# Kernel optimization log

Hardware: AMD Instinct MI355X
Metric: run time of the kernel (lower is better)

Reference implementation:

```python
import jax, jax.numpy as jnp
import numpy as np

N = 50000   # nodes
E = 600000  # edges
IN = 512    # in_channels
H = 128     # hidden_channels
B = 64      # graphs in batch
L = 4       # GatedGraphConv layers
VIEWS = [[0, 9, 10], [1, 2, 3], [4, 5, 6], [7, 8, 11, 12]]  # syntactic/sequential/semantic/discourse


def layer_norm(x, w, b, eps=1e-5):
    mu = x.mean(-1, keepdims=True)
    var = ((x - mu) ** 2).mean(-1, keepdims=True)
    return (x - mu) / jnp.sqrt(var + eps) * w + b


def setup_inputs() -> dict:
    key = jax.random.key(0)
    ks = jax.random.split(key, 32)
    p = lambda k, shape: (jax.random.normal(k, shape, jnp.float32) * 0.02)
    inp = {
        'x': jax.random.normal(ks[0], (N, IN), jnp.float32),
        'edge_index': jax.random.randint(ks[1], (2, E), 0, N, dtype=jnp.int32),
        'edge_type': jax.random.randint(ks[2], (E,), 0, 13, dtype=jnp.int32),
        'batch': jnp.sort(jax.random.randint(ks[3], (N,), 0, B, dtype=jnp.int32)),
        # input projection (Linear + LayerNorm)
        'proj_w': p(ks[4], (IN, H)), 'proj_b': p(ks[5], (H,)),
        'ln0_w': jnp.ones((H,), jnp.float32), 'ln0_b': jnp.zeros((H,), jnp.float32),
        # per-view GatedGraphConv: weight [views, layers, H, H] + GRUCell params [views, 3H, H]
        'ggnn_w': p(ks[6], (4, L, H, H)),
        'gru_wih': p(ks[7], (4, 3 * H, H)), 'gru_whh': p(ks[8], (4, 3 * H, H)),
        'gru_bih': p(ks[9], (4, 3 * H)), 'gru_bhh': p(ks[10], (4, 3 * H)),
        # per-view LayerNorm
        'vln_w': jnp.ones((4, H), jnp.float32), 'vln_b': jnp.zeros((4, H), jnp.float32),
        # attention fusion
        'q_w': p(ks[11], (H, H)), 'q_b': p(ks[12], (H,)),
        'k_w': p(ks[13], (H, H)), 'k_b': p(ks[14], (H,)),
        # classifier MLP: 2H -> H -> H//2 -> 1
        'c1_w': p(ks[15], (2 * H, H)), 'c1_b': p(ks[16], (H,)),
        'c2_w': p(ks[17], (H, H // 2)), 'c2_b': p(ks[18], (H // 2,)),
        'c3_w': p(ks[19], (H // 2, 1)), 'c3_b': p(ks[20], (1,)),
    }
    return inp


def reference(x, edge_index, edge_type, batch, proj_w, proj_b, ln0_w, ln0_b,
              ggnn_w, gru_wih, gru_whh, gru_bih, gru_bhh, vln_w, vln_b,
              q_w, q_b, k_w, k_b, c1_w, c1_b, c2_w, c2_b, c3_w, c3_b):
    # input projection: Linear -> LayerNorm -> GELU (dropout = identity in eval)
    h0 = jax.nn.gelu(layer_norm(x @ proj_w + proj_b, ln0_w, ln0_b), approximate=False)
    src, dst = edge_index[0], edge_index[1]
    views = []
    for v in range(4):
        emask = jnp.zeros((E,), bool)
        for t in VIEWS[v]:
            emask = emask | (edge_type == t)
        em = emask.astype(h0.dtype)[:, None]  # [E,1] edge-type view mask
        h = h0
        for i in range(L):
            m = h @ ggnn_w[v, i]                                   # [N,H]
            agg = jax.ops.segment_sum(m[src] * em, dst, num_segments=N)  # masked scatter-add
            # GRUCell(input=agg, hidden=h), torch gate order r,z,n
            gi = agg @ gru_wih[v].T + gru_bih[v]
            gh = h @ gru_whh[v].T + gru_bhh[v]
            ir, iz, inn = jnp.split(gi, 3, -1)
            hr, hz, hn = jnp.split(gh, 3, -1)
            r = jax.nn.sigmoid(ir + hr)
            z = jax.nn.sigmoid(iz + hz)
            n = jnp.tanh(inn + r * hn)
            h = (1.0 - z) * n + z * h
        views.append(layer_norm(h, vln_w[v], vln_b[v]) + h0)  # residual ViewEncoder
    hs = jnp.stack(views, 1)  # [N,4,H]
    # node-conditioned attention fusion
    q = jnp.tanh(h0 @ q_w + q_b)
    keys = hs @ k_w + k_b
    attn = jax.nn.softmax(jnp.einsum('nh,nvh->nv', q, keys) * (H ** -0.5), axis=-1)
    fused = jnp.einsum('nvh,nv->nh', hs, attn)
    # global mean + max pooling per graph
    cnt = jax.ops.segment_sum(jnp.ones((N,), fused.dtype), batch, num_segments=B)
    x_mean = jax.ops.segment_sum(fused, batch, num_segments=B) / jnp.maximum(cnt, 1.0)[:, None]
    x_max = jax.ops.segment_max(fused, batch, num_segments=B)
    g = jnp.concatenate([x_mean, x_max], -1)  # [B,2H]
    h1 = jax.nn.relu(g @ c1_w + c1_b)
    h2 = jax.nn.relu(h1 @ c2_w + c2_b)
    return h2 @ c3_w + c3_b  # [B,1] logits
```

## Files before the change

kernel.cpp:

```cpp
#include <hip/hip_runtime.h>
#include <math.h>


typedef __attribute__((ext_vector_type(8))) short short8;
typedef __attribute__((ext_vector_type(4))) float floatx4;

__device__ __forceinline__ unsigned short f2bf_rtn(float x) {
    unsigned u = __float_as_uint(x);
    return (unsigned short)((u + 0x7FFFu + ((u >> 16) & 1u)) >> 16);
}
__device__ __forceinline__ float bf2f(unsigned short h) {
    return __uint_as_float((unsigned)h << 16);
}
__device__ __forceinline__ float fsig(float x) {
    return __builtin_amdgcn_rcpf(1.0f + __expf(-x));
}
__device__ __forceinline__ float ftanh(float x) {
    return 1.0f - 2.0f * __builtin_amdgcn_rcpf(__expf(2.0f * x) + 1.0f);
}

__device__ __forceinline__ int view_of(int t) {
    return (t >= 1 && t <= 3) ? 1 : (t >= 4 && t <= 6) ? 2
         : ((t == 7) || (t == 8) || (t >= 11)) ? 3 : 0;
}

template <bool BT, int EPI>
__global__ __launch_bounds__(256, 2) void gemm_k(
    const float* __restrict__ A, const float* __restrict__ Bm,
    const float* __restrict__ bias, float* __restrict__ C,
    int N, int M, int K, long sA, long sB, long sC)
{
    __shared__ float As[32][132];
    __shared__ float Bs[32][132];
    A  += (long)blockIdx.z * sA;
    Bm += (long)blockIdx.z * sB;
    C  += (long)blockIdx.z * sC;
    const int r0 = blockIdx.x * 128;
    const int c0 = blockIdx.y * 128;
    const int tid = threadIdx.x;
    const int tx = tid & 15;
    const int ty = tid >> 4;

    float acc[8][8];
#pragma unroll
    for (int i = 0; i < 8; i++)
#pragma unroll
        for (int j = 0; j < 8; j++) acc[i][j] = 0.0f;

    for (int k0 = 0; k0 < K; k0 += 32) {
        {
            int arow = tid >> 3;
            int akq  = (tid & 7) << 2;
#pragma unroll
            for (int hh = 0; hh < 4; hh++) {
                int r  = arow + hh * 32;
                int gr = r0 + r;
                float4 av = make_float4(0.f, 0.f, 0.f, 0.f);
                if (gr < N) av = *(const float4*)(A + (long)gr * K + k0 + akq);
                As[akq + 0][r] = av.x; As[akq + 1][r] = av.y;
                As[akq + 2][r] = av.z; As[akq + 3][r] = av.w;
            }
        }
        if (BT) {
            int brow = tid >> 3;
            int bkq  = (tid & 7) << 2;
#pragma unroll
            for (int hh = 0; hh < 4; hh++) {
                int r = brow + hh * 32;
                float4 bv = *(const float4*)(Bm + (long)(c0 + r) * K + k0 + bkq);
                Bs[bkq + 0][r] = bv.x; Bs[bkq + 1][r] = bv.y;
                Bs[bkq + 2][r] = bv.z; Bs[bkq + 3][r] = bv.w;
            }
        } else {
            int kk0 = tid >> 5;
            int bmq = (tid & 31) << 2;
#pragma unroll
            for (int hh = 0; hh < 4; hh++) {
                int kk = kk0 + hh * 8;
                float4 bv = *(const float4*)(Bm + (long)(k0 + kk) * M + c0 + bmq);
                *(float4*)&Bs[kk][bmq] = bv;
            }
        }
        __syncthreads();
#pragma unroll
        for (int k = 0; k < 32; k++) {
            float4 a0 = *(const float4*)&As[k][ty << 2];
            float4 a1 = *(const float4*)&As[k][64 + (ty << 2)];
            float4 b0 = *(const float4*)&Bs[k][tx << 2];
            float4 b1 = *(const float4*)&Bs[k][64 + (tx << 2)];
            float av[8] = {a0.x, a0.y, a0.z, a0.w, a1.x, a1.y, a1.z, a1.w};
            float bv[8] = {b0.x, b0.y, b0.z, b0.w, b1.x, b1.y, b1.z, b1.w};
#pragma unroll
            for (int i = 0; i < 8; i++)
#pragma unroll
                for (int j = 0; j < 8; j++) acc[i][j] += av[i] * bv[j];
        }
        __syncthreads();
    }

    float bb[8] = {0, 0, 0, 0, 0, 0, 0, 0};
    if (bias) {
        float4 b0 = *(const float4*)(bias + c0 + (tx << 2));
        float4 b1 = *(const float4*)(bias + c0 + 64 + (tx << 2));
        bb[0] = b0.x; bb[1] = b0.y; bb[2] = b0.z; bb[3] = b0.w;
        bb[4] = b1.x; bb[5] = b1.y; bb[6] = b1.z; bb[7] = b1.w;
    }
#pragma unroll
    for (int i = 0; i < 8; i++) {
        int r = (i < 4) ? (r0 + (ty << 2) + i) : (r0 + 64 + (ty << 2) + i - 4);
        if (r < N) {
            float v[8];
#pragma unroll
            for (int j = 0; j < 8; j++) {
                v[j] = acc[i][j] + bb[j];
                if (EPI == 1) v[j] = tanhf(v[j]);
            }
            *(float4*)(C + (long)r * M + c0 + (tx << 2)) = make_float4(v[0], v[1], v[2], v[3]);
            *(float4*)(C + (long)r * M + c0 + 64 + (tx << 2)) = make_float4(v[4], v[5], v[6], v[7]);
        }
    }
}

__global__ __launch_bounds__(256) void build_p_k(
    const float* __restrict__ gwih, const float* __restrict__ gwhh,
    const float* __restrict__ gbih, const float* __restrict__ gbhh,
    float* __restrict__ pih, float* __restrict__ phh, float* __restrict__ bp)
{
    int idx = blockIdx.x * 256 + threadIdx.x;
    if (idx < 16 * 65536) {
        int z = idx >> 16, rem = idx & 65535;
        int k = rem >> 9, mcol = rem & 511;
        int ch = mcol >> 2, g = mcol & 3;
        int v = z >> 2;
        const float* Wih = gwih + (long)v * 384 * 128;
        float val = 0.0f;
        if (g == 0) val = Wih[ch * 128 + k];
        else if (g == 1) val = Wih[(128 + ch) * 128 + k];
        else if (g == 2) val = Wih[(256 + ch) * 128 + k];
        pih[idx] = val;
    }
    if (idx < 4 * 65536) {
        int v = idx >> 16, rem = idx & 65535;
        int k = rem >> 9, mcol = rem & 511;
        int ch = mcol >> 2, g = mcol & 3;
        const float* Whh = gwhh + (long)v * 384 * 128;
        float val = 0.0f;
        if (g == 0) val = Whh[ch * 128 + k];
        else if (g == 1) val = Whh[(128 + ch) * 128 + k];
        else if (g == 3) val = Whh[(256 + ch) * 128 + k];
        phh[idx] = val;
    }
    if (idx < 4 * 512) {
        int v = idx >> 9, mcol = idx & 511;
        int ch = mcol >> 2, g = mcol & 3;
        float val;
        if (g == 0) val = gbih[v * 384 + ch] + gbhh[v * 384 + ch];
        else if (g == 1) val = gbih[v * 384 + 128 + ch] + gbhh[v * 384 + 128 + ch];
        else if (g == 2) val = gbih[v * 384 + 256 + ch];
        else val = gbhh[v * 384 + 256 + ch];
        bp[idx] = val;
    }
}

__global__ __launch_bounds__(256) void pack_b_k(
    const float* __restrict__ wcomb, const float* __restrict__ phh,
    short* __restrict__ Bp)
{
    int idx = blockIdx.x * 256 + threadIdx.x;
    if (idx >= 16 * 256 * 512) return;
    int z = idx >> 17, rem = idx & 131071;
    int k = rem >> 9, col = rem & 511;
    int g  = col & 3;
    int q  = (col >> 2) & 3;
    int tn = (col >> 4) & 7;
    int ch = ((col >> 7) << 5) + (q << 3) + tn;
    int mcol = (ch << 2) + g;
    float val = (k < 128) ? wcomb[(long)z * 65536 + k * 512 + mcol]
                          : phh[(long)(z >> 2) * 65536 + (k - 128) * 512 + mcol];
    long dst = ((long)(z * 8 + (k >> 5)) * 512 + col) * 32 + ((k >> 3) & 3) * 8 + (k & 7);
    Bp[dst] = (short)f2bf_rtn(val);
}

template <bool BT>
__global__ __launch_bounds__(256) void pack_w_k(
    const float* __restrict__ W, short* __restrict__ bhi, short* __restrict__ blo, int K)
{
    int idx = blockIdx.x * 256 + threadIdx.x;
    if (idx >= K * 128) return;
    int k = idx >> 7, col = idx & 127;
    float v = BT ? W[col * K + k] : W[k * 128 + col];
    unsigned short h = f2bf_rtn(v);
    float fh = __uint_as_float((unsigned)h << 16);
    long dst = ((long)(k >> 5) * 128 + col) * 32 + ((k >> 3) & 3) * 8 + (k & 7);
    bhi[dst] = (short)h;
    blo[dst] = (short)f2bf_rtn(v - fh);
}

template <int EPI>
__global__ __launch_bounds__(256, 4) void gemm_mfma_k(
    const float* __restrict__ A, const short* __restrict__ Bhi,
    const short* __restrict__ Blo, const float* __restrict__ bias,
    float* __restrict__ C, int N, int K)
{
    __shared__ __align__(16) short Ahi[64 * 40];
    __shared__ __align__(16) short Alo[64 * 40];
    const int r0 = blockIdx.x * 64;
    const int tid = threadIdx.x;
    const int l = tid & 63, w = tid >> 6;
    const int wrow = w * 16;
    const int m = l & 15, q = l >> 4;

    floatx4 acc[8];
#pragma unroll
    for (int b = 0; b < 8; b++) acc[b] = (floatx4)0.0f;

    const int arow = tid >> 2;
    const int fcol = (tid & 3) * 8;
    const int gr = r0 + arow;
    const int nks = K >> 5;

    for (int ks = 0; ks < nks; ks++) {
        float xv[8];
        if (gr < N) {
            float4 x0 = *(const float4*)(A + (long)gr * K + ks * 32 + fcol);
            float4 x1 = *(const float4*)(A + (long)gr * K + ks * 32 + fcol + 4);
            xv[0] = x0.x; xv[1] = x0.y; xv[2] = x0.z; xv[3] = x0.w;
            xv[4] = x1.x; xv[5] = x1.y; xv[6] = x1.z; xv[7] = x1.w;
        } else {
#pragma unroll
            for (int u = 0; u < 8; u++) xv[u] = 0.0f;
        }
        short8 vhi, vlo;
#pragma unroll
        for (int u = 0; u < 8; u++) {
            unsigned short hb = f2bf_rtn(xv[u]);
            float fh = __uint_as_float((unsigned)hb << 16);
            vhi[u] = (short)hb;
            vlo[u] = (short)f2bf_rtn(xv[u] - fh);
        }
        *(short8*)&Ahi[arow * 40 + fcol] = vhi;
        *(short8*)&Alo[arow * 40 + fcol] = vlo;
        __syncthreads();
        short8 ah = *(short8*)&Ahi[(wrow + m) * 40 + q * 8];
        short8 al = *(short8*)&Alo[(wrow + m) * 40 + q * 8];
#pragma unroll
        for (int tn = 0; tn < 8; tn++) {
            int col = tn * 16 + m;
            short8 bh = *(const short8*)(Bhi + ((long)ks * 128 + col) * 32 + q * 8);
            short8 bl = *(const short8*)(Blo + ((long)ks * 128 + col) * 32 + q * 8);
            acc[tn] = __builtin_amdgcn_mfma_f32_16x16x32_bf16(ah, bh, acc[tn], 0, 0, 0);
            acc[tn] = __builtin_amdgcn_mfma_f32_16x16x32_bf16(al, bh, acc[tn], 0, 0, 0);
            acc[tn] = __builtin_amdgcn_mfma_f32_16x16x32_bf16(ah, bl, acc[tn], 0, 0, 0);
        }
        __syncthreads();
    }

#pragma unroll
    for (int tn = 0; tn < 8; tn++) {
        int col = tn * 16 + m;
        float bb = bias ? bias[col] : 0.0f;
#pragma unroll
        for (int reg = 0; reg < 4; reg++) {
            int row = r0 + wrow + q * 4 + reg;
            if (row < N) {
                float v = acc[tn][reg] + bb;
                if (EPI == 1) v = ftanh(v);
                C[(long)row * 128 + col] = v;
            }
        }
    }
}

__global__ __launch_bounds__(512, 4) void gemm_gru_mfma_k(
    const short* __restrict__ hb, const short* __restrict__ hpHi,
    const short* __restrict__ hpLo, const short* __restrict__ Bp,
    const float* __restrict__ bp, short* __restrict__ outHi,
    short* __restrict__ outLo, const int* __restrict__ off,
    const int* __restrict__ esrc, int N, long sV, long sHb, long sHp)
{
    __shared__ __align__(16) short As[8 * 64 * 40];
    const int x = blockIdx.x;
    const int z = blockIdx.z;
    const short* hbz = hb + (long)z * sHb;
    const short* hph = hpHi + (long)z * sHp;
    const short* hpl = hpLo + (long)z * sHp;
    Bp  += (long)z * 524288;
    bp  += (long)z * 512;
    outHi += (long)z * sV;
    outLo += (long)z * sV;
    const int r0  = x * 64;
    const int tid = threadIdx.x;
    const int l = tid & 63, w = tid >> 6;
    const int wrow = (w & 1) * 32, wcol = (w >> 1) * 128;
    const int m = l & 15, q = l >> 4;

    const int row8 = tid >> 3;
    const int cg8  = tid & 7;
    const int gr = r0 + row8;

    {
        float accS[16];
#pragma unroll
        for (int u = 0; u < 16; u++) accS[u] = 0.0f;
        if (gr < N) {
            const int idx = z * N + gr;
            int j = off[idx];
            const int end = off[idx + 1];
            if (j < end) {
                const short* sp = hb + (long)esrc[j] * 128 + (cg8 << 4);
                short8 p0 = *(const short8*)(sp);
                short8 p1 = *(const short8*)(sp + 8);
                for (; j < end;) {
                    short8 c0 = p0, c1 = p1;
                    ++j;
                    if (j < end) {
                        const short* sq = hb + (long)esrc[j] * 128 + (cg8 << 4);
                        p0 = *(const short8*)(sq);
                        p1 = *(const short8*)(sq + 8);
                    }
#pragma unroll
                    for (int u = 0; u < 8; u++) {
                        accS[u]     += bf2f((unsigned short)c0[u]);
                        accS[8 + u] += bf2f((unsigned short)c1[u]);
                    }
                }
            }
        }
        short8 o0, o1;
#pragma unroll
        for (int u = 0; u < 8; u++) {
            o0[u] = (short)f2bf_rtn(accS[u]);
            o1[u] = (short)f2bf_rtn(accS[8 + u]);
        }
        const int base = (cg8 >> 1) * 2560 + row8 * 40 + (cg8 & 1) * 16;
        *(short8*)&As[base]     = o0;
        *(short8*)&As[base + 8] = o1;
    }

    {
        short8 h0v = (short8)0, h1v = (short8)0;
        if (gr < N) {
            const short* hp = hbz + (long)gr * 128 + (cg8 << 4);
            h0v = *(const short8*)(hp);
            h1v = *(const short8*)(hp + 8);
        }
        const int base = (4 + (cg8 >> 1)) * 2560 + row8 * 40 + (cg8 & 1) * 16;
        *(short8*)&As[base]     = h0v;
        *(short8*)&As[base + 8] = h1v;
    }
    __syncthreads();

    floatx4 acc[2][8];
#pragma unroll
    for (int a = 0; a < 2; a++)
#pragma unroll
        for (int b = 0; b < 8; b++) acc[a][b] = (floatx4)0.0f;

#pragma unroll
    for (int ks = 0; ks < 8; ks++) {
        short8 bfr[8];
#pragma unroll
        for (int tn = 0; tn < 8; tn++) {
            int col = wcol + tn * 16 + m;
            bfr[tn] = *(const short8*)(Bp + ((long)ks * 512 + col) * 32 + q * 8);
        }
        short8 a0 = *(short8*)&As[ks * 2560 + (wrow + m) * 40 + q * 8];
        short8 a1 = *(short8*)&As[ks * 2560 + (wrow + 16 + m) * 40 + q * 8];
#pragma unroll
        for (int tn = 0; tn < 8; tn++) {
            acc[0][tn] = __builtin_amdgcn_mfma_f32_16x16x32_bf16(bfr[tn], a0, acc[0][tn], 0, 0, 0);
            acc[1][tn] = __builtin_amdgcn_mfma_f32_16x16x32_bf16(bfr[tn], a1, acc[1][tn], 0, 0, 0);
        }
    }

    const int chq = (wcol >> 2) + q * 8;
#pragma unroll
    for (int a = 0; a < 2; a++) {
        const int row = r0 + wrow + a * 16 + m;
        if (row < N) {
            short8 h8 = *(const short8*)(hph + (long)row * 128 + chq);
            short8 l8 = *(const short8*)(hpl + (long)row * 128 + chq);
            float hnv[8];
            short8 ohi, olo;
#pragma unroll
            for (int tn = 0; tn < 8; tn++) {
                float hp = bf2f((unsigned short)h8[tn]) + bf2f((unsigned short)l8[tn]);
                float4 bv = *(const float4*)(bp + (chq + tn) * 4);
                floatx4 A = acc[a][tn];
                float rr = fsig(A[0] + bv.x);
                float zz = fsig(A[1] + bv.y);
                float nn = ftanh(A[2] + bv.z + rr * (A[3] + bv.w));
                hnv[tn] = (1.0f - zz) * nn + zz * hp;
                unsigned short hh = f2bf_rtn(hnv[tn]);
                ohi[tn] = (short)hh;
                olo[tn] = (short)f2bf_rtn(hnv[tn] - bf2f(hh));
            }
            *(short8*)(outHi + (long)row * 128 + chq) = ohi;
            *(short8*)(outLo + (long)row * 128 + chq) = olo;
        }
    }
}

__global__ __launch_bounds__(256) void ln_gelu_k(
    float* __restrict__ h0, short* __restrict__ h0b, short* __restrict__ h0lo,
    const float* __restrict__ w, const float* __restrict__ b, int N)
{
    long t = (long)blockIdx.x * 256 + threadIdx.x;
    int n = (int)(t >> 5), lane = (int)(t & 31);
    if (n >= N) return;
    float* p = h0 + (long)n * 128 + lane * 4;
    float4 x = *(float4*)p;
    float s = x.x + x.y + x.z + x.w;
#pragma unroll
    for (int off = 16; off >= 1; off >>= 1) s += __shfl_xor(s, off);
    float mu = s * (1.0f / 128.0f);
    float4 d = make_float4(x.x - mu, x.y - mu, x.z - mu, x.w - mu);
    float ss = d.x * d.x + d.y * d.y + d.z * d.z + d.w * d.w;
#pragma unroll
    for (int off = 16; off >= 1; off >>= 1) ss += __shfl_xor(ss, off);
    float inv = 1.0f / sqrtf(ss * (1.0f / 128.0f) + 1e-5f);
    float4 wv = *(const float4*)(w + lane * 4);
    float4 bv = *(const float4*)(b + lane * 4);
    float y[4] = {d.x * inv * wv.x + bv.x, d.y * inv * wv.y + bv.y,
                  d.z * inv * wv.z + bv.z, d.w * inv * wv.w + bv.w};
#pragma unroll
    for (int i = 0; i < 4; i++)
        y[i] = 0.5f * y[i] * (1.0f + erff(y[i] * 0.70710678118654752f));
    *(float4*)p = make_float4(y[0], y[1], y[2], y[3]);
    ushort4 hb, lb;
    hb.x = f2bf_rtn(y[0]); lb.x = f2bf_rtn(y[0] - bf2f(hb.x));
    hb.y = f2bf_rtn(y[1]); lb.y = f2bf_rtn(y[1] - bf2f(hb.y));
    hb.z = f2bf_rtn(y[2]); lb.z = f2bf_rtn(y[2] - bf2f(hb.z));
    hb.w = f2bf_rtn(y[3]); lb.w = f2bf_rtn(y[3] - bf2f(hb.w));
    *(ushort4*)(h0b + (long)n * 128 + lane * 4) = hb;
    *(ushort4*)(h0lo + (long)n * 128 + lane * 4) = lb;
}

__global__ __launch_bounds__(256) void count_k(
    const int* __restrict__ dst, const int* __restrict__ et,
    int* __restrict__ cnt, int E, int N)
{
    int e = blockIdx.x * 256 + threadIdx.x;
    if (e >= E) return;
    int v = view_of(et[e]);
    atomicAdd(&cnt[v * N + dst[e]], 1);
}

__global__ __launch_bounds__(256) void scan1_k(
    const int* __restrict__ cnt, int* __restrict__ off, int* __restrict__ bsum, int n)
{
    __shared__ int sm[256];
    int base = blockIdx.x * 1024;
    int tid = threadIdx.x;
    int v[4]; int s = 0;
#pragma unroll
    for (int i = 0; i < 4; i++) {
        int idx = base + tid * 4 + i;
        v[i] = (idx < n) ? cnt[idx] : 0; s += v[i];
    }
    sm[tid] = s; __syncthreads();
    for (int o = 1; o < 256; o <<= 1) {
        int t2 = (tid >= o) ? sm[tid - o] : 0;
        __syncthreads(); sm[tid] += t2; __syncthreads();
    }
    int run = sm[tid] - s;
    if (tid == 255) bsum[blockIdx.x] = sm[255];
#pragma unroll
    for (int i = 0; i < 4; i++) {
        int idx = base + tid * 4 + i;
        if (idx < n) off[idx] = run;
        run += v[i];
    }
}

__global__ __launch_bounds__(256) void scan2_k(int* __restrict__ bsum, int nb)
{
    __shared__ int sm[256];
    int tid = threadIdx.x;
    int v = (tid < nb) ? bsum[tid] : 0;
    sm[tid] = v; __syncthreads();
    for (int o = 1; o < 256; o <<= 1) {
        int t2 = (tid >= o) ? sm[tid - o] : 0;
        __syncthreads(); sm[tid] += t2; __syncthreads();
    }
    if (tid < nb) bsum[tid] = sm[tid] - v;
}

__global__ __launch_bounds__(256) void scan3_k(
    int* __restrict__ off, int* __restrict__ cursor,
    const int* __restrict__ bsum, int n, int total)
{
    int i = blockIdx.x * 256 + threadIdx.x;
    if (i < n) {
        int o = off[i] + bsum[i >> 10];
        off[i] = o; cursor[i] = o;
    }
    if (i == 0) off[n] = total;
}

__global__ __launch_bounds__(256) void fill_k(
    const int* __restrict__ src, const int* __restrict__ dst,
    const int* __restrict__ et, int* __restrict__ cursor,
    int* __restrict__ esrc, int* __restrict__ esrc0, int E, int N)
{
    int e = blockIdx.x * 256 + threadIdx.x;
    if (e >= E) return;
    int v = view_of(et[e]);
    int b = v * N + dst[e];
    int pos = atomicAdd(&cursor[b], 1);
    esrc[pos] = v * N + src[e];
    esrc0[pos] = src[e];
}

__global__ __launch_bounds__(256) void fusion_k(
    const short* __restrict__ hi, const short* __restrict__ lo,
    const float* __restrict__ h0, const float* __restrict__ q,
    const float* __restrict__ u, const float* __restrict__ kb,
    const float* __restrict__ vw, const float* __restrict__ vb,
    float* __restrict__ fused, int N)
{
    long t = (long)blockIdx.x * 256 + threadIdx.x;
    int n = (int)(t >> 5), lane = (int)(t & 31);
    if (n >= N) return;
    float4 qv = *(const float4*)(q + (long)n * 128 + lane * 4);
    float4 kv = *(const float4*)(kb + lane * 4);
    float4 uv = *(const float4*)(u + (long)n * 128 + lane * 4);
    float4 h0v = *(const float4*)(h0 + (long)n * 128 + lane * 4);
    float part = qv.x * kv.x + qv.y * kv.y + qv.z * kv.z + qv.w * kv.w;
    float hs[4][4];
    float lg[4];
#pragma unroll
    for (int v = 0; v < 4; v++) {
        long base = ((long)v * N + n) * 128 + lane * 4;
        ushort4 hu = *(const ushort4*)(hi + base);
        ushort4 lu = *(const ushort4*)(lo + base);
        float hv0 = bf2f(hu.x) + bf2f(lu.x);
        float hv1 = bf2f(hu.y) + bf2f(lu.y);
        float hv2 = bf2f(hu.z) + bf2f(lu.z);
        float hv3 = bf2f(hu.w) + bf2f(lu.w);
        float s = hv0 + hv1 + hv2 + hv3;
#pragma unroll
        for (int off = 16; off >= 1; off >>= 1) s += __shfl_xor(s, off);
        float mu = s * (1.0f / 128.0f);
        float d0 = hv0 - mu, d1 = hv1 - mu, d2 = hv2 - mu, d3 = hv3 - mu;
        float ss = d0 * d0 + d1 * d1 + d2 * d2 + d3 * d3;
#pragma unroll
        for (int off = 16; off >= 1; off >>= 1) ss += __shfl_xor(ss, off);
        float inv = 1.0f / sqrtf(ss * (1.0f / 128.0f) + 1e-5f);
        float4 wv = *(const float4*)(vw + v * 128 + lane * 4);
        float4 bv = *(const float4*)(vb + v * 128 + lane * 4);
        hs[v][0] = d0 * inv * wv.x + bv.x + h0v.x;
        hs[v][1] = d1 * inv * wv.y + bv.y + h0v.y;
        hs[v][2] = d2 * inv * wv.z + bv.z + h0v.z;
        hs[v][3] = d3 * inv * wv.w + bv.w + h0v.w;
        lg[v] = hs[v][0] * uv.x + hs[v][1] * uv.y + hs[v][2] * uv.z + hs[v][3] * uv.w;
    }
#pragma unroll
    for (int off = 16; off >= 1; off >>= 1) {
        part += __shfl_xor(part, off);
#pragma unroll
        for (int v = 0; v < 4; v++) lg[v] += __shfl_xor(lg[v], off);
    }
    const float scale = 0.08838834764831845f;
    float mx = -1e30f;
#pragma unroll
    for (int v = 0; v < 4; v++) { lg[v] = (lg[v] + part) * scale; mx = fmaxf(mx, lg[v]); }
    float se = 0.0f;
#pragma unroll
    for (int v = 0; v < 4; v++) { lg[v] = expf(lg[v] - mx); se += lg[v]; }
    float inv = 1.0f / se;
    float4 f = make_float4(0.f, 0.f, 0.f, 0.f);
#pragma unroll
    for (int v = 0; v < 4; v++) {
        float a = lg[v] * inv;
        f.x += a * hs[v][0]; f.y += a * hs[v][1];
        f.z += a * hs[v][2]; f.w += a * hs[v][3];
    }
    *(float4*)(fused + (long)n * 128 + lane * 4) = f;
}

__global__ __launch_bounds__(256) void pool_k(
    const float* __restrict__ fused, const int* __restrict__ batch,
    float* __restrict__ meanb, float* __restrict__ maxb, int N)
{
    __shared__ float s_sum[256], s_max[256];
    int b = blockIdx.x;
    int lo = 0, hi = N;
    while (lo < hi) { int mid = (lo + hi) >> 1; if (batch[mid] < b) lo = mid + 1; else hi = mid; }
    int beg = lo;
    lo = beg; hi = N;
    while (lo < hi) { int mid = (lo + hi) >> 1; if (batch[mid] < b + 1) lo = mid + 1; else hi = mid; }
    int end = lo;
    int tid = threadIdx.x;
    int c = tid & 127, half = tid >> 7;
    float sum = 0.0f, mx = __int_as_float(0xff800000);
    for (int n = beg + half; n < end; n += 2) {
        float v = fused[(long)n * 128 + c];
        sum += v; mx = fmaxf(mx, v);
    }
    s_sum[tid] = sum; s_max[tid] = mx;
    __syncthreads();
    if (half == 0) {
        float tot = s_sum[tid] + s_sum[tid + 128];
        float m2 = fmaxf(s_max[tid], s_max[tid + 128]);
        int cnt = end - beg;
        meanb[b * 128 + c] = tot / (float)max(cnt, 1);
        maxb[b * 128 + c] = m2;
    }
}

__global__ __launch_bounds__(256) void classifier_k(
    const float* __restrict__ meanb, const float* __restrict__ maxb,
    const float* __restrict__ c1w, const float* __restrict__ c1b,
    const float* __restrict__ c2w, const float* __restrict__ c2b,
    const float* __restrict__ c3w, const float* __restrict__ c3b,
    float* __restrict__ out)
{
    __shared__ float g[256];
    __shared__ float h1[128];
    __shared__ float h2[64];
    int b = blockIdx.x, tid = threadIdx.x;
    g[tid] = (tid < 128) ? meanb[b * 128 + tid] : maxb[b * 128 + (tid - 128)];
    __syncthreads();
    if (tid < 128) {
        float acc = c1b[tid];
        for (int k = 0; k < 256; k++) acc += g[k] * c1w[k * 128 + tid];
        h1[tid] = fmaxf(acc, 0.0f);
    }
    __syncthreads();
    if (tid < 64) {
        float acc = c2b[tid];
        for (int k = 0; k < 128; k++) acc += h1[k] * c2w[k * 64 + tid];
        h2[tid] = fmaxf(acc, 0.0f);
    }
    __syncthreads();
    if (tid < 64) {
        float p = h2[tid] * c3w[tid];
#pragma unroll
        for (int off = 32; off >= 1; off >>= 1) p += __shfl_xor(p, off);
        if (tid == 0) out[b] = c3b[0] + p;
    }
}

extern "C" void kernel_launch(void* const* d_in, const int* in_sizes, int n_in,
                              void* d_out, int out_size, void* d_ws, size_t ws_size,
                              hipStream_t stream) {
    (void)n_in; (void)out_size; (void)ws_size;
    const float* x      = (const float*)d_in[0];
    const int*   eidx   = (const int*)d_in[1];
    const int*   etype  = (const int*)d_in[2];
    const int*   batch  = (const int*)d_in[3];
    const float* proj_w = (const float*)d_in[4];
    const float* proj_b = (const float*)d_in[5];
    const float* ln0_w  = (const float*)d_in[6];
    const float* ln0_b  = (const float*)d_in[7];
    const float* ggnn_w = (const float*)d_in[8];
    const float* gwih   = (const float*)d_in[9];
    const float* gwhh   = (const float*)d_in[10];
    const float* gbih   = (const float*)d_in[11];
    const float* gbhh   = (const float*)d_in[12];
    const float* vln_w  = (const float*)d_in[13];
    const float* vln_b  = (const float*)d_in[14];
    const float* q_w    = (const float*)d_in[15];
    const float* q_b    = (const float*)d_in[16];
    const float* k_w    = (const float*)d_in[17];
    const float* k_b    = (const float*)d_in[18];
    const float* c1w    = (const float*)d_in[19];
    const float* c1b    = (const float*)d_in[20];
    const float* c2w    = (const float*)d_in[21];
    const float* c2b    = (const float*)d_in[22];
    const float* c3w    = (const float*)d_in[23];
    const float* c3b    = (const float*)d_in[24];
    float* out = (float*)d_out;

    const int N = in_sizes[3];
    const int E = in_sizes[2];
    const int IN = in_sizes[0] / N;
    const int H = 128, L = 4;
    const int N4 = 4 * N;

    long NH = (long)N * H;
    float* ws = (float*)d_ws;
    float* h0 = ws;
    float* hfz = h0 + NH;
    short* loA = (short*)hfz;
    short* loB = loA + 4 * NH;
    float* poolMean = hfz + 4 * NH;
    float* poolMax  = poolMean + 8192;
    float* bp = poolMax + 8192;
    short* h0b = (short*)(bp + 2048);
    short* hiA = h0b + NH;
    short* hiB = hiA + 4 * NH;
    short* Sb  = hiB + 4 * NH;
    short* Bp  = Sb + 4 * NH;
    short* prjHi = Bp + 16 * 131072;
    short* prjLo = prjHi + 65536;
    short* qwHi  = prjLo + 65536;
    short* qwLo  = qwHi + 16384;
    short* kwHi  = qwLo + 16384;
    short* kwLo  = kwHi + 16384;
    int* iOff  = (int*)(kwLo + 16384);
    int* iCnt  = iOff + N4 + 1;
    int* iCur  = iCnt + N4;
    int* iBsum = iCur + N4;
    int* iEsrc  = iBsum + 256;
    int* iEsrc0 = iEsrc + E;
    float* wcomb = hfz;
    float* pih   = hfz + 16 * 65536;
    float* phh   = pih + 16 * 65536;
    short* lo0 = loB;
    float* qbuf  = (float*)Sb;
    float* ubuf  = qbuf + NH;
    float* fused = (float*)hiA;

    int rb = (int)(((long)N * 32 + 255) / 256);
    int eb = (E + 255) / 256;
    int nbScan = (N4 + 1023) / 1024;
    int gx64 = (N + 63) / 64;

    const int* esrc_in = eidx;
    const int* edst_in = eidx + E;

    hipMemsetAsync(iCnt, 0, (size_t)N4 * sizeof(int), stream);
    count_k<<<eb, 256, 0, stream>>>(edst_in, etype, iCnt, E, N);
    scan1_k<<<nbScan, 256, 0, stream>>>(iCnt, iOff, iBsum, N4);
    scan2_k<<<1, 256, 0, stream>>>(iBsum, nbScan);
    scan3_k<<<(N4 + 255) / 256, 256, 0, stream>>>(iOff, iCur, iBsum, N4, E);
    fill_k<<<eb, 256, 0, stream>>>(esrc_in, edst_in, etype, iCur, iEsrc, iEsrc0, E, N);

    build_p_k<<<(16 * 65536 + 255) / 256, 256, 0, stream>>>(
        gwih, gwhh, gbih, gbhh, pih, phh, bp);
    gemm_k<false, 0><<<dim3(1, 4, 16), 256, 0, stream>>>(
        ggnn_w, pih, nullptr, wcomb, 128, 512, 128,
        (long)H * H, 65536, 65536);
    pack_b_k<<<(16 * 256 * 512 + 255) / 256, 256, 0, stream>>>(wcomb, phh, Bp);
    pack_w_k<false><<<(IN * 128 + 255) / 256, 256, 0, stream>>>(proj_w, prjHi, prjLo, IN);
    pack_w_k<false><<<(128 * 128 + 255) / 256, 256, 0, stream>>>(q_w, qwHi, qwLo, 128);
    pack_w_k<true><<<(128 * 128 + 255) / 256, 256, 0, stream>>>(k_w, kwHi, kwLo, 128);

    gemm_mfma_k<0><<<gx64, 256, 0, stream>>>(x, prjHi, prjLo, proj_b, h0, N, IN);
    ln_gelu_k<<<rb, 256, 0, stream>>>(h0, h0b, lo0, ln0_w, ln0_b, N);

    const short* hin = h0b;  long sHb = 0;
    const short* hpH = h0b;  const short* hpL = lo0;  long sHp = 0;
    short* oHi = hiA; short* oLo = loA;
    for (int i = 0; i < L; i++) {
        const int* es = (i == 0) ? iEsrc0 : iEsrc;
        gemm_gru_mfma_k<<<dim3(gx64, 1, 4), 512, 0, stream>>>(
            hin, hpH, hpL, Bp + (long)i * 131072, bp, oHi, oLo, iOff, es,
            N, NH, sHb, sHp);
        hpH = oHi; hpL = oLo; sHp = NH;
        hin = oHi; sHb = NH;
        if (oHi == hiA) { oHi = hiB; oLo = loB; }
        else            { oHi = hiA; oLo = loA; }
    }

    gemm_mfma_k<1><<<gx64, 256, 0, stream>>>(h0, qwHi, qwLo, q_b, qbuf, N, 128);
    gemm_mfma_k<0><<<gx64, 256, 0, stream>>>(qbuf, kwHi, kwLo, nullptr, ubuf, N, 128);
    fusion_k<<<rb, 256, 0, stream>>>(hiB, loB, h0, qbuf, ubuf, k_b,
                                     vln_w, vln_b, fused, N);
    pool_k<<<64, 256, 0, stream>>>(fused, batch, poolMean, poolMax, N);
    classifier_k<<<64, 256, 0, stream>>>(
        poolMean, poolMax, c1w, c1b, c2w, c2b, c3w, c3b, out);
}
```

Baseline: 1.246 ms.

## Fuse input projection GEMM with LayerNorm+GELU epilogue; coalesce B packing writes

Adds a projection GEMM kernel whose epilogue performs the row LayerNorm and GELU in registers via lane shuffles, then writes h0 in fp32 plus bf16 hi/lo splits directly. This removes the separate ln_gelu pass and its fp32 round trip of h0. The B-packing kernel is also reindexed so each thread writes contiguous destination addresses, with scattered reads instead of scattered writes. The fused epilogue does strided scalar stores instead of vectorized ones and uses a 4-waves-per-EU launch bound that may constrain registers.

Result: no change. 1.224 ms (-1.8%).

```diff
diff --git a/kernel.cpp b/kernel.cpp
--- a/kernel.cpp
+++ b/kernel.cpp
@@ -166,10 +166,14 @@
     const float* __restrict__ wcomb, const float* __restrict__ phh,
     short* __restrict__ Bp)
 {
-    int idx = blockIdx.x * 256 + threadIdx.x;
-    if (idx >= 16 * 256 * 512) return;
-    int z = idx >> 17, rem = idx & 131071;
-    int k = rem >> 9, col = rem & 511;
+    long d = (long)blockIdx.x * 256 + threadIdx.x;
+    if (d >= (long)16 * 256 * 512) return;
+    int j   = (int)(d & 7);
+    int sub = (int)((d >> 3) & 3);
+    int col = (int)((d >> 5) & 511);
+    int zk  = (int)(d >> 14);
+    int ks  = zk & 7, z = zk >> 3;
+    int k = ks * 32 + sub * 8 + j;
     int g  = col & 3;
     int q  = (col >> 2) & 3;
     int tn = (col >> 4) & 7;
@@ -177,8 +181,7 @@
     int mcol = (ch << 2) + g;
     float val = (k < 128) ? wcomb[(long)z * 65536 + k * 512 + mcol]
                           : phh[(long)(z >> 2) * 65536 + (k - 128) * 512 + mcol];
-    long dst = ((long)(z * 8 + (k >> 5)) * 512 + col) * 32 + ((k >> 3) & 3) * 8 + (k & 7);
-    Bp[dst] = (short)f2bf_rtn(val);
+    Bp[d] = (short)f2bf_rtn(val);
 }
 
 template <bool BT>
@@ -266,6 +269,111 @@
                 float v = acc[tn][reg] + bb;
                 if (EPI == 1) v = ftanh(v);
                 C[(long)row * 128 + col] = v;
+            }
+        }
+    }
+}
+
+__global__ __launch_bounds__(256, 4) void gemm_proj_ln_k(
+    const float* __restrict__ A, const short* __restrict__ Bhi,
+    const short* __restrict__ Blo, const float* __restrict__ bias,
+    const float* __restrict__ lnw, const float* __restrict__ lnb,
+    float* __restrict__ h0, short* __restrict__ h0b, short* __restrict__ h0lo,
+    int N, int K)
+{
+    __shared__ __align__(16) short Ahi[64 * 40];
+    __shared__ __align__(16) short Alo[64 * 40];
+    const int r0 = blockIdx.x * 64;
+    const int tid = threadIdx.x;
+    const int l = tid & 63, w = tid >> 6;
+    const int wrow = w * 16;
+    const int m = l & 15, q = l >> 4;
+
+    floatx4 acc[8];
+#pragma unroll
+    for (int b = 0; b < 8; b++) acc[b] = (floatx4)0.0f;
+
+    const int arow = tid >> 2;
+    const int fcol = (tid & 3) * 8;
+    const int gr = r0 + arow;
+    const int nks = K >> 5;
+
+    for (int ks = 0; ks < nks; ks++) {
+        float xv[8];
+        if (gr < N) {
+            float4 x0 = *(const float4*)(A + (long)gr * K + ks * 32 + fcol);
+            float4 x1 = *(const float4*)(A + (long)gr * K + ks * 32 + fcol + 4);
+            xv[0] = x0.x; xv[1] = x0.y; xv[2] = x0.z; xv[3] = x0.w;
+            xv[4] = x1.x; xv[5] = x1.y; xv[6] = x1.z; xv[7] = x1.w;
+        } else {
+#pragma unroll
+            for (int u = 0; u < 8; u++) xv[u] = 0.0f;
+        }
+        short8 vhi, vlo;
+#pragma unroll
+        for (int u = 0; u < 8; u++) {
+            unsigned short hb = f2bf_rtn(xv[u]);
+            float fh = __uint_as_float((unsigned)hb << 16);
+            vhi[u] = (short)hb;
+            vlo[u] = (short)f2bf_rtn(xv[u] - fh);
+        }
+        *(short8*)&Ahi[arow * 40 + fcol] = vhi;
+        *(short8*)&Alo[arow * 40 + fcol] = vlo;
+        __syncthreads();
+        short8 ah = *(short8*)&Ahi[(wrow + m) * 40 + q * 8];
+        short8 al = *(short8*)&Alo[(wrow + m) * 40 + q * 8];
+#pragma unroll
+        for (int tn = 0; tn < 8; tn++) {
+            int col = tn * 16 + m;
+            short8 bh = *(const short8*)(Bhi + ((long)ks * 128 + col) * 32 + q * 8);
+            short8 bl = *(const short8*)(Blo + ((long)ks * 128 + col) * 32 + q * 8);
+            acc[tn] = __builtin_amdgcn_mfma_f32_16x16x32_bf16(ah, bh, acc[tn], 0, 0, 0);
+            acc[tn] = __builtin_amdgcn_mfma_f32_16x16x32_bf16(al, bh, acc[tn], 0, 0, 0);
+            acc[tn] = __builtin_amdgcn_mfma_f32_16x16x32_bf16(ah, bl, acc[tn], 0, 0, 0);
+        }
+        __syncthreads();
+    }
+
+    float bb[8], lw[8], lb[8];
+#pragma unroll
+    for (int tn = 0; tn < 8; tn++) {
+        int col = tn * 16 + m;
+        bb[tn] = bias[col];
+        lw[tn] = lnw[col];
+        lb[tn] = lnb[col];
+    }
+#pragma unroll
+    for (int reg = 0; reg < 4; reg++) {
+        const int row = r0 + wrow + q * 4 + reg;
+        float v8[8];
+        float s = 0.0f;
+#pragma unroll
+        for (int tn = 0; tn < 8; tn++) {
+            v8[tn] = acc[tn][reg] + bb[tn];
+            s += v8[tn];
+        }
+#pragma unroll
+        for (int off = 8; off >= 1; off >>= 1) s += __shfl_xor(s, off);
+        float mu = s * (1.0f / 128.0f);
+        float ss = 0.0f;
+#pragma unroll
+        for (int tn = 0; tn < 8; tn++) {
+            float d = v8[tn] - mu;
+            ss += d * d;
+        }
+#pragma unroll
+        for (int off = 8; off >= 1; off >>= 1) ss += __shfl_xor(ss, off);
+        float inv = 1.0f / sqrtf(ss * (1.0f / 128.0f) + 1e-5f);
+        if (row < N) {
+#pragma unroll
+            for (int tn = 0; tn < 8; tn++) {
+                int col = tn * 16 + m;
+                float y = (v8[tn] - mu) * inv * lw[tn] + lb[tn];
+                y = 0.5f * y * (1.0f + erff(y * 0.70710678118654752f));
+                h0[(long)row * 128 + col] = y;
+                unsigned short hh = f2bf_rtn(y);
+                h0b[(long)row * 128 + col] = (short)hh;
+                h0lo[(long)row * 128 + col] = (short)f2bf_rtn(y - bf2f(hh));
             }
         }
     }
@@ -399,41 +507,6 @@
             *(short8*)(outLo + (long)row * 128 + chq) = olo;
         }
     }
-}
-
-__global__ __launch_bounds__(256) void ln_gelu_k(
-    float* __restrict__ h0, short* __restrict__ h0b, short* __restrict__ h0lo,
-    const float* __restrict__ w, const float* __restrict__ b, int N)
-{
-    long t = (long)blockIdx.x * 256 + threadIdx.x;
-    int n = (int)(t >> 5), lane = (int)(t & 31);
-    if (n >= N) return;
-    float* p = h0 + (long)n * 128 + lane * 4;
-    float4 x = *(float4*)p;
-    float s = x.x + x.y + x.z + x.w;
-#pragma unroll
-    for (int off = 16; off >= 1; off >>= 1) s += __shfl_xor(s, off);
-    float mu = s * (1.0f / 128.0f);
-    float4 d = make_float4(x.x - mu, x.y - mu, x.z - mu, x.w - mu);
-    float ss = d.x * d.x + d.y * d.y + d.z * d.z + d.w * d.w;
-#pragma unroll
-    for (int off = 16; off >= 1; off >>= 1) ss += __shfl_xor(ss, off);
-    float inv = 1.0f / sqrtf(ss * (1.0f / 128.0f) + 1e-5f);
-    float4 wv = *(const float4*)(w + lane * 4);
-    float4 bv = *(const float4*)(b + lane * 4);
-    float y[4] = {d.x * inv * wv.x + bv.x, d.y * inv * wv.y + bv.y,
-                  d.z * inv * wv.z + bv.z, d.w * inv * wv.w + bv.w};
-#pragma unroll
-    for (int i = 0; i < 4; i++)
-        y[i] = 0.5f * y[i] * (1.0f + erff(y[i] * 0.70710678118654752f));
-    *(float4*)p = make_float4(y[0], y[1], y[2], y[3]);
-    ushort4 hb, lb;
-    hb.x = f2bf_rtn(y[0]); lb.x = f2bf_rtn(y[0] - bf2f(hb.x));
-    hb.y = f2bf_rtn(y[1]); lb.y = f2bf_rtn(y[1] - bf2f(hb.y));
-    hb.z = f2bf_rtn(y[2]); lb.z = f2bf_rtn(y[2] - bf2f(hb.z));
-    hb.w = f2bf_rtn(y[3]); lb.w = f2bf_rtn(y[3] - bf2f(hb.w));
-    *(ushort4*)(h0b + (long)n * 128 + lane * 4) = hb;
-    *(ushort4*)(h0lo + (long)n * 128 + lane * 4) = lb;
 }
 
 __global__ __launch_bounds__(256) void count_k(
@@ -738,8 +811,8 @@
     pack_w_k<false><<<(128 * 128 + 255) / 256, 256, 0, stream>>>(q_w, qwHi, qwLo, 128);
     pack_w_k<true><<<(128 * 128 + 255) / 256, 256, 0, stream>>>(k_w, kwHi, kwLo, 128);
 
-    gemm_mfma_k<0><<<gx64, 256, 0, stream>>>(x, prjHi, prjLo, proj_b, h0, N, IN);
-    ln_gelu_k<<<rb, 256, 0, stream>>>(h0, h0b, lo0, ln0_w, ln0_b, N);
+    gemm_proj_ln_k<<<gx64, 256, 0, stream>>>(
+        x, prjHi, prjLo, proj_b, ln0_w, ln0_b, h0, h0b, lo0, N, IN);
 
     const short* hin = h0b;  long sHb = 0;
     const short* hpH = h0b;  const short* hpL = lo0;  long sHp = 0;
```
